# Optimization experiments

Hardware: AMD Instinct MI355X
Metric: run time of the kernel (lower is better)

## Reference

```python
import jax, jax.numpy as jnp
import numpy as np


def _patch_points(P):
    # replicates: meshgrid(y,x,z, indexing='ij'); points = cat([zz, yy, xx], -1).reshape(-1,3)
    lin = jnp.linspace(-1.0, 1.0, P)
    a, b, c = jnp.meshgrid(lin, lin, lin, indexing='ij')  # all identical linspaces
    pts = jnp.stack([c, b, a], axis=-1).reshape(-1, 3)     # (P^3, 3)
    return pts


def _proj_locations(points, angles):
    # Tomographic projection geometry (generate_projections_location):
    # rotate points about the detector-vertical axis and keep in-plane coords.
    # points: (N,3); angles: (A,) radians. Returns (A, N, 2) grid coords (x, y)
    # in grid_sample convention (last dim: x indexes width, y indexes height).
    p0 = points[:, 0]
    p1 = points[:, 1]
    p2 = points[:, 2]
    c = jnp.cos(angles)[:, None]   # (A,1)
    s = jnp.sin(angles)[:, None]
    gx = p0[None, :] * c + p2[None, :] * s          # (A, N)
    gy = jnp.broadcast_to(p1[None, :], gx.shape)    # (A, N)
    return jnp.stack([gx, gy], axis=-1)             # (A, N, 2)


def _bilinear_sample(img, grid):
    # img: (C,H,W); grid: (N,2) in [-1,1], align_corners=True, padding zeros.
    C, H, W = img.shape
    ix = (grid[:, 0] + 1.0) * 0.5 * (W - 1)
    iy = (grid[:, 1] + 1.0) * 0.5 * (H - 1)
    ix0 = jnp.floor(ix)
    iy0 = jnp.floor(iy)
    ix1 = ix0 + 1.0
    iy1 = iy0 + 1.0
    wx1 = ix - ix0
    wx0 = 1.0 - wx1
    wy1 = iy - iy0
    wy0 = 1.0 - wy1

    def corner(iyc, ixc, w):
        valid = (ixc >= 0) & (ixc <= W - 1) & (iyc >= 0) & (iyc <= H - 1)
        xi = jnp.clip(ixc, 0, W - 1).astype(jnp.int32)
        yi = jnp.clip(iyc, 0, H - 1).astype(jnp.int32)
        return img[:, yi, xi] * (w * valid)[None, :]   # (C,N)

    return (corner(iy0, ix0, wy0 * wx0) + corner(iy0, ix1, wy0 * wx1)
            + corner(iy1, ix0, wy1 * wx0) + corner(iy1, ix1, wy1 * wx1))


def setup_inputs() -> dict:
    key = jax.random.key(0)
    k1, k2 = jax.random.split(key)
    B, A, P = 128, 121, 33
    x = jax.random.normal(k1, (B, A, P, P), dtype=jnp.float32)
    angles = jax.random.uniform(k2, (1, A), dtype=jnp.float32,
                                minval=0.0, maxval=2.0 * np.pi)
    return {"x": x, "angles": angles}


def reference(x, angles):
    B, A, P, _ = x.shape
    pts = _patch_points(P)                       # (P^3, 3)
    grids = _proj_locations(pts, angles[0])      # (A, P^3, 2)
    xs = jnp.transpose(x, (1, 0, 2, 3))          # (A, B, P, P)

    def body(acc, inp):
        xi, gi = inp                             # (B,P,P), (P^3,2)
        return acc + _bilinear_sample(xi, gi), None

    acc0 = jnp.zeros((B, P * P * P), dtype=x.dtype)
    acc, _ = jax.lax.scan(body, acc0, (xs, grids))
    x_fbp = acc.reshape(B, P, P, P) / A
    return x_fbp
```

## Files before the change

kernel.cpp:

```cpp
#include <hip/hip_runtime.h>
#include <hip/hip_fp16.h>
#include <math.h>


#define PDIM 33
#define PP   1089
#define A_   121
#define K_   3993
#define KP   4032
#define MP   1152
#define MT2  18
#define NT2  66
#define OUTB 35937

typedef _Float16 f16x8 __attribute__((ext_vector_type(8)));
typedef float    f32x4 __attribute__((ext_vector_type(4)));

typedef __attribute__((address_space(1))) const unsigned int* gp_t;
typedef __attribute__((address_space(3))) unsigned int*       lp_t;


__global__ __launch_bounds__(128)
void wfill_kernel(const float* __restrict__ angles, __half* __restrict__ W)
{
    const int n = blockIdx.x;
    const int t = threadIdx.x;
    __half* row = W + (size_t)n * KP;
    for (int e = t; e < KP; e += 128) row[e] = __float2half_rn(0.0f);
    __syncthreads();
    if (n >= PP || t >= A_) return;
    const int j  = t;
    const int i0 = n / PDIM;
    const int i2 = n - i0 * PDIM;
    float s, c;
    sincosf(angles[j], &s, &c);
    float ix = fmaf((float)(i2 - 16), c, fmaf((float)(i0 - 16), s, 16.0f));
    float fl = floorf(ix);
    int   k0 = (int)fl;
    float w1 = ix - fl;
    float w0 = 1.0f - w1;
    __half* seg = row + j * PDIM;
    if (k0 >= 0     && k0 < PDIM)     seg[k0]     = __float2half_rn(w0);
    if (k0 + 1 >= 0 && k0 + 1 < PDIM) seg[k0 + 1] = __float2half_rn(w1);
}

__global__ __launch_bounds__(256)
void xt_kernel(const float* __restrict__ x, __half* __restrict__ Xt)
{
    const int n  = blockIdx.x;
    const int i1 = n >> 7;
    const int b  = n & 127;
    const float* src = x + (size_t)b * (A_ * PP) + (size_t)i1 * PDIM;
    unsigned int* dst = (unsigned int*)(Xt + (size_t)n * KP);
    for (int e = threadIdx.x; e < KP / 2; e += 256) {
        int kk0 = 2 * e, kk1 = 2 * e + 1;
        float v0 = 0.0f, v1 = 0.0f;
        if (kk0 < K_) {
            int j = kk0 / PDIM, k = kk0 - j * PDIM;
            v0 = src[(size_t)j * PP + k];
        }
        if (kk1 < K_) {
            int j = kk1 / PDIM, k = kk1 - j * PDIM;
            v1 = src[(size_t)j * PP + k];
        }
        dst[e] = __builtin_bit_cast(unsigned int,
                     __builtin_amdgcn_cvt_pkrtz(v0, v1));
    }
}

__global__ __launch_bounds__(256)
void gemm_kernel(const __half* __restrict__ W, const __half* __restrict__ Xt,
                 float* __restrict__ out, float invA)
{
    __shared__ _Float16 As[64 * 64];
    __shared__ _Float16 Bs[64 * 64];

    const int blk   = blockIdx.x;
    const int tileN = blk / MT2;
    const int tileM = blk - tileN * MT2;
    const int t     = threadIdx.x;
    const int lane  = t & 63;
    const int wave  = t >> 6;
    const int warpM = wave >> 1;
    const int warpN = wave & 1;
    const int quad  = lane >> 4;
    const int l15   = lane & 15;

    f32x4 acc[2][2] = {};

    const __half* Ab = W  + (size_t)(tileM * 64) * KP;
    const __half* Bb = Xt + (size_t)(tileN * 64) * KP;

    int srow[2], ssego[2];
#pragma unroll
    for (int i = 0; i < 2; ++i) {
        int cidx = t + i * 256;
        int row  = cidx >> 3;
        int seg  = cidx & 7;
        srow[i]  = row;
        ssego[i] = (seg ^ (row & 7)) * 8;
    }

    int arow[2], brow[2];
#pragma unroll
    for (int s = 0; s < 2; ++s) {
        arow[s] = warpM * 32 + s * 16 + l15;
        brow[s] = warpN * 32 + s * 16 + l15;
    }

    for (int kb = 0; kb < KP; kb += 64) {
        __syncthreads();
#pragma unroll
        for (int i = 0; i < 2; ++i) {
            const __half* ga = Ab + (size_t)srow[i] * KP + kb + ssego[i];
            const __half* gb = Bb + (size_t)srow[i] * KP + kb + ssego[i];
            __builtin_amdgcn_global_load_lds((gp_t)(const void*)ga,
                (lp_t)(void*)&As[(t + i * 256) * 8], 16, 0, 0);
            __builtin_amdgcn_global_load_lds((gp_t)(const void*)gb,
                (lp_t)(void*)&Bs[(t + i * 256) * 8], 16, 0, 0);
        }
        __syncthreads();

        f16x8 af[2][2], bf[2][2];
#pragma unroll
        for (int h = 0; h < 2; ++h) {
#pragma unroll
            for (int s = 0; s < 2; ++s) {
                int ks = h * 4 + quad;
                af[h][s] = *(const f16x8*)&As[arow[s] * 64 + ((ks ^ (arow[s] & 7)) * 8)];
                bf[h][s] = *(const f16x8*)&Bs[brow[s] * 64 + ((ks ^ (brow[s] & 7)) * 8)];
            }
        }
#pragma unroll
        for (int h = 0; h < 2; ++h)
#pragma unroll
            for (int ms = 0; ms < 2; ++ms)
#pragma unroll
                for (int ns = 0; ns < 2; ++ns)
                    acc[ms][ns] = __builtin_amdgcn_mfma_f32_16x16x32_f16(
                        af[h][ms], bf[h][ns], acc[ms][ns], 0, 0, 0);
    }

#pragma unroll
    for (int ns = 0; ns < 2; ++ns) {
        int nglob = tileN * 64 + warpN * 32 + ns * 16 + l15;
        int i1 = nglob >> 7;
        int b  = nglob & 127;
        float* ob = out + (size_t)b * OUTB + (size_t)i1 * PDIM;
#pragma unroll
        for (int ms = 0; ms < 2; ++ms) {
#pragma unroll
            for (int r = 0; r < 4; ++r) {
                int m = tileM * 64 + warpM * 32 + ms * 16 + quad * 4 + r;
                if (m < PP) {
                    int i0 = m / PDIM;
                    int i2 = m - i0 * PDIM;
                    ob[(size_t)i0 * PP + i2] = acc[ms][ns][r] * invA;
                }
            }
        }
    }
}


#define ROWW 47
#define PADL 7
#define BLK  384
#define NV   3
#define GRID 1280

typedef _Float16 h2v __attribute__((ext_vector_type(2)));

#if defined(__has_builtin)
#if __has_builtin(__builtin_amdgcn_fractf)
#define FRACTF(x) __builtin_amdgcn_fractf(x)
#endif
#endif
#ifndef FRACTF
#define FRACTF(x) ((x) - floorf(x))
#endif

__device__ __forceinline__ float fdot2u(unsigned int a, unsigned int b, float c)
{
    return __builtin_amdgcn_fdot2(__builtin_bit_cast(h2v, a),
                                  __builtin_bit_cast(h2v, b), c, false);
}

__global__ __launch_bounds__(BLK)
void fbp_adjoint_kernel(const float* __restrict__ x,
                        const float* __restrict__ angles,
                        float* __restrict__ out,
                        int nslice, float invA)
{
    __shared__ unsigned int dr[A_ * ROWW];
    __shared__ float2       cs_lds[A_];

    const int t = threadIdx.x;
    for (int j = t; j < A_; j += BLK) {
        float s, c;
        sincosf(angles[j], &s, &c);
        cs_lds[j] = make_float2(c, s);
    }

    float u0[NV], u2[NV];
#pragma unroll
    for (int nn = 0; nn < NV; ++nn) {
        int n  = t + nn * BLK;
        int nc = (n < PP) ? n : (PP - 1);
        int q0 = nc / PDIM;
        int q2 = nc - q0 * PDIM;
        u0[nn] = (float)(q0 - 16);
        u2[nn] = (float)(q2 - 16);
    }

    for (int slice = blockIdx.x; slice < nslice; slice += GRID) {
        if (slice != (int)blockIdx.x) __syncthreads();
        const int hb = slice / PDIM;
        const int i1 = slice - hb * PDIM;
        const int b0 = 2 * hb;
        const float* r0 = x + (size_t)b0 * (A_ * PP) + (size_t)i1 * PDIM;
        const float* r1 = r0 + (size_t)(A_ * PP);
        for (int e = t; e < A_ * ROWW; e += BLK) {
            int j = e / ROWW;
            int p = e - j * ROWW;
            int k = p - PADL;
            float f0 = 0.0f, f1 = 0.0f;
            if (k >= 0 && k < PDIM) {
                size_t o = (size_t)j * PP + k;
                f0 = r0[o];
                f1 = r1[o];
            }
            dr[e] = __builtin_bit_cast(unsigned int,
                        __halves2half2(__float2half_rn(f0), __float2half_rn(f1)));
        }
        __syncthreads();

        float a0[NV] = {0.0f, 0.0f, 0.0f};
        float a1[NV] = {0.0f, 0.0f, 0.0f};
#pragma unroll 2
        for (int j = 0; j < A_; ++j) {
            float2 cj = cs_lds[j];
            const unsigned int* base = &dr[j * ROWW];
#pragma unroll
            for (int nn = 0; nn < NV; ++nn) {
                float ixp = fmaf(u2[nn], cj.x, fmaf(u0[nn], cj.y, 23.0f));
                int   kp  = (int)ixp;
                float w1  = FRACTF(ixp);
                unsigned int wp = __builtin_bit_cast(unsigned int,
                                    __builtin_amdgcn_cvt_pkrtz(1.0f - w1, w1));
                unsigned int d0 = base[kp];
                unsigned int d1 = base[kp + 1];
                unsigned int p0 = __builtin_amdgcn_perm(d1, d0, 0x05040100u);
                unsigned int p1 = __builtin_amdgcn_perm(d1, d0, 0x07060302u);
                a0[nn] = fdot2u(p0, wp, a0[nn]);
                a1[nn] = fdot2u(p1, wp, a1[nn]);
            }
        }

        float* ob0 = out + (size_t)b0 * OUTB + (size_t)i1 * PDIM;
        float* ob1 = ob0 + (size_t)OUTB;
#pragma unroll
        for (int nn = 0; nn < NV; ++nn) {
            int n = t + nn * BLK;
            if (n < PP) {
                int q0 = n / PDIM;
                int q2 = n - q0 * PDIM;
                size_t o = (size_t)q0 * PP + q2;
                ob0[o] = a0[nn] * invA;
                ob1[o] = a1[nn] * invA;
            }
        }
    }
}


extern "C" void kernel_launch(void* const* d_in, const int* in_sizes, int n_in,
                              void* d_out, int out_size, void* d_ws, size_t ws_size,
                              hipStream_t stream)
{
    const float* x      = (const float*)d_in[0];
    const float* angles = (const float*)d_in[1];
    float* out          = (float*)d_out;

    const int A = in_sizes[1];
    const int B = in_sizes[0] / (A * PP);
    const float invA = 1.0f / (float)A;

    const size_t wBytes  = (size_t)MP * KP * sizeof(__half);
    const size_t xtBytes = (size_t)(PDIM * B) * KP * sizeof(__half);

    if (ws_size >= wBytes + xtBytes && A == A_ && B == 128) {
        __half* W  = (__half*)d_ws;
        __half* Xt = (__half*)((char*)d_ws + wBytes);
        wfill_kernel<<<MP, 128, 0, stream>>>(angles, W);
        xt_kernel<<<PDIM * B, 256, 0, stream>>>(x, Xt);
        gemm_kernel<<<NT2 * MT2, 256, 0, stream>>>(W, Xt, out, invA);
    } else {
        const int nslice = (B / 2) * PDIM;
        dim3 grid(GRID < nslice ? GRID : nslice);
        fbp_adjoint_kernel<<<grid, BLK, 0, stream>>>(x, angles, out,
                                                     nslice, invA);
    }
}
```

Measured before the change: 191.5 us.

## Double-buffer GEMM LDS tiles and merge prep kernels into one launch

Result: slower. 199.0 us (+4.0%).

```diff
diff --git a/kernel.cpp b/kernel.cpp
--- a/kernel.cpp
+++ b/kernel.cpp
@@ -20,51 +20,54 @@
 typedef __attribute__((address_space(3))) unsigned int*       lp_t;
 
 
-__global__ __launch_bounds__(128)
-void wfill_kernel(const float* __restrict__ angles, __half* __restrict__ W)
-{
-    const int n = blockIdx.x;
-    const int t = threadIdx.x;
-    __half* row = W + (size_t)n * KP;
-    for (int e = t; e < KP; e += 128) row[e] = __float2half_rn(0.0f);
-    __syncthreads();
-    if (n >= PP || t >= A_) return;
-    const int j  = t;
-    const int i0 = n / PDIM;
-    const int i2 = n - i0 * PDIM;
-    float s, c;
-    sincosf(angles[j], &s, &c);
-    float ix = fmaf((float)(i2 - 16), c, fmaf((float)(i0 - 16), s, 16.0f));
-    float fl = floorf(ix);
-    int   k0 = (int)fl;
-    float w1 = ix - fl;
-    float w0 = 1.0f - w1;
-    __half* seg = row + j * PDIM;
-    if (k0 >= 0     && k0 < PDIM)     seg[k0]     = __float2half_rn(w0);
-    if (k0 + 1 >= 0 && k0 + 1 < PDIM) seg[k0 + 1] = __float2half_rn(w1);
-}
-
 __global__ __launch_bounds__(256)
-void xt_kernel(const float* __restrict__ x, __half* __restrict__ Xt)
-{
-    const int n  = blockIdx.x;
-    const int i1 = n >> 7;
-    const int b  = n & 127;
-    const float* src = x + (size_t)b * (A_ * PP) + (size_t)i1 * PDIM;
-    unsigned int* dst = (unsigned int*)(Xt + (size_t)n * KP);
-    for (int e = threadIdx.x; e < KP / 2; e += 256) {
-        int kk0 = 2 * e, kk1 = 2 * e + 1;
-        float v0 = 0.0f, v1 = 0.0f;
-        if (kk0 < K_) {
-            int j = kk0 / PDIM, k = kk0 - j * PDIM;
-            v0 = src[(size_t)j * PP + k];
-        }
-        if (kk1 < K_) {
-            int j = kk1 / PDIM, k = kk1 - j * PDIM;
-            v1 = src[(size_t)j * PP + k];
-        }
-        dst[e] = __builtin_bit_cast(unsigned int,
-                     __builtin_amdgcn_cvt_pkrtz(v0, v1));
+void prep_kernel(const float* __restrict__ x, const float* __restrict__ angles,
+                 __half* __restrict__ Xt, __half* __restrict__ W)
+{
+    const int blk = blockIdx.x;
+    const int t   = threadIdx.x;
+
+    if (blk < PDIM * 128) {
+        const int n  = blk;
+        const int i1 = n >> 7;
+        const int b  = n & 127;
+        const float* src = x + (size_t)b * (A_ * PP) + (size_t)i1 * PDIM;
+        unsigned int* dst = (unsigned int*)(Xt + (size_t)n * KP);
+        for (int e = t; e < KP / 2; e += 256) {
+            int kk0 = 2 * e, kk1 = 2 * e + 1;
+            float v0 = 0.0f, v1 = 0.0f;
+            if (kk0 < K_) {
+                int j = kk0 / PDIM, k = kk0 - j * PDIM;
+                v0 = src[(size_t)j * PP + k];
+            }
+            if (kk1 < K_) {
+                int j = kk1 / PDIM, k = kk1 - j * PDIM;
+                v1 = src[(size_t)j * PP + k];
+            }
+            dst[e] = __builtin_bit_cast(unsigned int,
+                         __builtin_amdgcn_cvt_pkrtz(v0, v1));
+        }
+    } else {
+        const int n = blk - PDIM * 128;
+        __half* row = W + (size_t)n * KP;
+        int4 zz = make_int4(0, 0, 0, 0);
+        for (int e = t; e < KP / 8; e += 256)
+            ((int4*)row)[e] = zz;
+        __syncthreads();
+        if (n >= PP || t >= A_) return;
+        const int j  = t;
+        const int i0 = n / PDIM;
+        const int i2 = n - i0 * PDIM;
+        float s, c;
+        sincosf(angles[j], &s, &c);
+        float ix = fmaf((float)(i2 - 16), c, fmaf((float)(i0 - 16), s, 16.0f));
+        float fl = floorf(ix);
+        int   k0 = (int)fl;
+        float w1 = ix - fl;
+        float w0 = 1.0f - w1;
+        __half* seg = row + j * PDIM;
+        if (k0 >= 0     && k0 < PDIM)     seg[k0]     = __float2half_rn(w0);
+        if (k0 + 1 >= 0 && k0 + 1 < PDIM) seg[k0 + 1] = __float2half_rn(w1);
     }
 }
 
@@ -72,8 +75,8 @@
 void gemm_kernel(const __half* __restrict__ W, const __half* __restrict__ Xt,
                  float* __restrict__ out, float invA)
 {
-    __shared__ _Float16 As[64 * 64];
-    __shared__ _Float16 Bs[64 * 64];
+    __shared__ _Float16 As[2][64 * 64];
+    __shared__ _Float16 Bs[2][64 * 64];
 
     const int blk   = blockIdx.x;
     const int tileN = blk / MT2;
@@ -108,27 +111,29 @@
         brow[s] = warpN * 32 + s * 16 + l15;
     }
 
-    for (int kb = 0; kb < KP; kb += 64) {
-        __syncthreads();
+    auto stage = [&](int sel, int kb) {
 #pragma unroll
         for (int i = 0; i < 2; ++i) {
             const __half* ga = Ab + (size_t)srow[i] * KP + kb + ssego[i];
             const __half* gb = Bb + (size_t)srow[i] * KP + kb + ssego[i];
             __builtin_amdgcn_global_load_lds((gp_t)(const void*)ga,
-                (lp_t)(void*)&As[(t + i * 256) * 8], 16, 0, 0);
+                (lp_t)(void*)&As[sel][(t + i * 256) * 8], 16, 0, 0);
             __builtin_amdgcn_global_load_lds((gp_t)(const void*)gb,
-                (lp_t)(void*)&Bs[(t + i * 256) * 8], 16, 0, 0);
-        }
-        __syncthreads();
-
+                (lp_t)(void*)&Bs[sel][(t + i * 256) * 8], 16, 0, 0);
+        }
+    };
+
+    auto compute = [&](int sel) {
         f16x8 af[2][2], bf[2][2];
 #pragma unroll
         for (int h = 0; h < 2; ++h) {
 #pragma unroll
             for (int s = 0; s < 2; ++s) {
                 int ks = h * 4 + quad;
-                af[h][s] = *(const f16x8*)&As[arow[s] * 64 + ((ks ^ (arow[s] & 7)) * 8)];
-                bf[h][s] = *(const f16x8*)&Bs[brow[s] * 64 + ((ks ^ (brow[s] & 7)) * 8)];
+                af[h][s] = *(const f16x8*)
+                    &As[sel][arow[s] * 64 + ((ks ^ (arow[s] & 7)) * 8)];
+                bf[h][s] = *(const f16x8*)
+                    &Bs[sel][brow[s] * 64 + ((ks ^ (brow[s] & 7)) * 8)];
             }
         }
 #pragma unroll
@@ -139,7 +144,32 @@
                 for (int ns = 0; ns < 2; ++ns)
                     acc[ms][ns] = __builtin_amdgcn_mfma_f32_16x16x32_f16(
                         af[h][ms], bf[h][ns], acc[ms][ns], 0, 0, 0);
-    }
+    };
+
+    stage(0, 0);
+    for (int kb = 64; kb + 64 < KP; kb += 128) {
+        stage(1, kb);
+        asm volatile("s_waitcnt vmcnt(4)" ::: "memory");
+        __builtin_amdgcn_s_barrier();
+        asm volatile("" ::: "memory");
+        compute(0);
+        asm volatile("" ::: "memory");
+        __builtin_amdgcn_s_barrier();
+        asm volatile("" ::: "memory");
+
+        stage(0, kb + 64);
+        asm volatile("s_waitcnt vmcnt(4)" ::: "memory");
+        __builtin_amdgcn_s_barrier();
+        asm volatile("" ::: "memory");
+        compute(1);
+        asm volatile("" ::: "memory");
+        __builtin_amdgcn_s_barrier();
+        asm volatile("" ::: "memory");
+    }
+    asm volatile("s_waitcnt vmcnt(0)" ::: "memory");
+    __builtin_amdgcn_s_barrier();
+    asm volatile("" ::: "memory");
+    compute(0);
 
 #pragma unroll
     for (int ns = 0; ns < 2; ++ns) {
@@ -292,8 +322,7 @@
     if (ws_size >= wBytes + xtBytes && A == A_ && B == 128) {
         __half* W  = (__half*)d_ws;
         __half* Xt = (__half*)((char*)d_ws + wBytes);
-        wfill_kernel<<<MP, 128, 0, stream>>>(angles, W);
-        xt_kernel<<<PDIM * B, 256, 0, stream>>>(x, Xt);
+        prep_kernel<<<PDIM * B + MP, 256, 0, stream>>>(x, angles, Xt, W);
         gemm_kernel<<<NT2 * MT2, 256, 0, stream>>>(W, Xt, out, invA);
     } else {
         const int nslice = (B / 2) * PDIM;
```

## Split GEMM K dimension in two, merge prep kernels, add reduction pass

Applied to the files above, without the earlier changes.

Measured after the change: 211.3 us. +10.4%, slower.

```diff
diff --git a/kernel.cpp b/kernel.cpp
--- a/kernel.cpp
+++ b/kernel.cpp
@@ -8,6 +8,7 @@
 #define A_   121
 #define K_   3993
 #define KP   4032
+#define KSPL 2048
 #define MP   1152
 #define MT2  18
 #define NT2  66
@@ -20,62 +21,73 @@
 typedef __attribute__((address_space(3))) unsigned int*       lp_t;
 
 
-__global__ __launch_bounds__(128)
-void wfill_kernel(const float* __restrict__ angles, __half* __restrict__ W)
-{
-    const int n = blockIdx.x;
-    const int t = threadIdx.x;
-    __half* row = W + (size_t)n * KP;
-    for (int e = t; e < KP; e += 128) row[e] = __float2half_rn(0.0f);
-    __syncthreads();
-    if (n >= PP || t >= A_) return;
-    const int j  = t;
-    const int i0 = n / PDIM;
-    const int i2 = n - i0 * PDIM;
-    float s, c;
-    sincosf(angles[j], &s, &c);
-    float ix = fmaf((float)(i2 - 16), c, fmaf((float)(i0 - 16), s, 16.0f));
-    float fl = floorf(ix);
-    int   k0 = (int)fl;
-    float w1 = ix - fl;
-    float w0 = 1.0f - w1;
-    __half* seg = row + j * PDIM;
-    if (k0 >= 0     && k0 < PDIM)     seg[k0]     = __float2half_rn(w0);
-    if (k0 + 1 >= 0 && k0 + 1 < PDIM) seg[k0 + 1] = __float2half_rn(w1);
-}
-
 __global__ __launch_bounds__(256)
-void xt_kernel(const float* __restrict__ x, __half* __restrict__ Xt)
-{
-    const int n  = blockIdx.x;
-    const int i1 = n >> 7;
-    const int b  = n & 127;
-    const float* src = x + (size_t)b * (A_ * PP) + (size_t)i1 * PDIM;
-    unsigned int* dst = (unsigned int*)(Xt + (size_t)n * KP);
-    for (int e = threadIdx.x; e < KP / 2; e += 256) {
-        int kk0 = 2 * e, kk1 = 2 * e + 1;
-        float v0 = 0.0f, v1 = 0.0f;
-        if (kk0 < K_) {
-            int j = kk0 / PDIM, k = kk0 - j * PDIM;
-            v0 = src[(size_t)j * PP + k];
-        }
-        if (kk1 < K_) {
-            int j = kk1 / PDIM, k = kk1 - j * PDIM;
-            v1 = src[(size_t)j * PP + k];
-        }
-        dst[e] = __builtin_bit_cast(unsigned int,
-                     __builtin_amdgcn_cvt_pkrtz(v0, v1));
+void prep_kernel(const float* __restrict__ x, const float* __restrict__ angles,
+                 __half* __restrict__ Xt, __half* __restrict__ W)
+{
+    const int blk = blockIdx.x;
+    const int t   = threadIdx.x;
+
+    if (blk < PDIM * 128) {
+        const int n  = blk;
+        const int i1 = n >> 7;
+        const int b  = n & 127;
+        const float* src = x + (size_t)b * (A_ * PP) + (size_t)i1 * PDIM;
+        unsigned int* dst = (unsigned int*)(Xt + (size_t)n * KP);
+        for (int e = t; e < KP / 2; e += 256) {
+            int kk0 = 2 * e, kk1 = 2 * e + 1;
+            float v0 = 0.0f, v1 = 0.0f;
+            if (kk0 < K_) {
+                int j = kk0 / PDIM, k = kk0 - j * PDIM;
+                v0 = src[(size_t)j * PP + k];
+            }
+            if (kk1 < K_) {
+                int j = kk1 / PDIM, k = kk1 - j * PDIM;
+                v1 = src[(size_t)j * PP + k];
+            }
+            dst[e] = __builtin_bit_cast(unsigned int,
+                         __builtin_amdgcn_cvt_pkrtz(v0, v1));
+        }
+    } else {
+        const int n = blk - PDIM * 128;
+        __half* row = W + (size_t)n * KP;
+        int4 zz = make_int4(0, 0, 0, 0);
+        for (int e = t; e < KP / 8; e += 256)
+            ((int4*)row)[e] = zz;
+        __syncthreads();
+        if (n >= PP || t >= A_) return;
+        const int j  = t;
+        const int i0 = n / PDIM;
+        const int i2 = n - i0 * PDIM;
+        float s, c;
+        sincosf(angles[j], &s, &c);
+        float ix = fmaf((float)(i2 - 16), c, fmaf((float)(i0 - 16), s, 16.0f));
+        float fl = floorf(ix);
+        int   k0 = (int)fl;
+        float w1 = ix - fl;
+        float w0 = 1.0f - w1;
+        __half* seg = row + j * PDIM;
+        if (k0 >= 0     && k0 < PDIM)     seg[k0]     = __float2half_rn(w0);
+        if (k0 + 1 >= 0 && k0 + 1 < PDIM) seg[k0 + 1] = __float2half_rn(w1);
     }
 }
 
 __global__ __launch_bounds__(256)
 void gemm_kernel(const __half* __restrict__ W, const __half* __restrict__ Xt,
-                 float* __restrict__ out, float invA)
+                 float* __restrict__ out, float* __restrict__ part,
+                 float scale)
 {
     __shared__ _Float16 As[64 * 64];
     __shared__ _Float16 Bs[64 * 64];
 
-    const int blk   = blockIdx.x;
+    int blk = blockIdx.x;
+    int kb0 = 0, kb1 = KP;
+    float* dst = out;
+    if (part) {
+        if (blk >= MT2 * NT2) { blk -= MT2 * NT2; dst = part; kb0 = KSPL; }
+        else                  { kb1 = KSPL; }
+    }
+
     const int tileN = blk / MT2;
     const int tileM = blk - tileN * MT2;
     const int t     = threadIdx.x;
@@ -108,7 +120,7 @@
         brow[s] = warpN * 32 + s * 16 + l15;
     }
 
-    for (int kb = 0; kb < KP; kb += 64) {
+    for (int kb = kb0; kb < kb1; kb += 64) {
         __syncthreads();
 #pragma unroll
         for (int i = 0; i < 2; ++i) {
@@ -146,7 +158,7 @@
         int nglob = tileN * 64 + warpN * 32 + ns * 16 + l15;
         int i1 = nglob >> 7;
         int b  = nglob & 127;
-        float* ob = out + (size_t)b * OUTB + (size_t)i1 * PDIM;
+        float* ob = dst + (size_t)b * OUTB + (size_t)i1 * PDIM;
 #pragma unroll
         for (int ms = 0; ms < 2; ++ms) {
 #pragma unroll
@@ -155,10 +167,29 @@
                 if (m < PP) {
                     int i0 = m / PDIM;
                     int i2 = m - i0 * PDIM;
-                    ob[(size_t)i0 * PP + i2] = acc[ms][ns][r] * invA;
+                    ob[(size_t)i0 * PP + i2] = acc[ms][ns][r] * scale;
                 }
             }
         }
+    }
+}
+
+__global__ __launch_bounds__(256)
+void reduce_kernel(float* __restrict__ out, const float* __restrict__ part,
+                   float invA)
+{
+    const int n4 = (128 * OUTB) / 4;
+    float4* o4 = (float4*)out;
+    const float4* p4 = (const float4*)part;
+    for (int e = blockIdx.x * 256 + threadIdx.x; e < n4;
+         e += gridDim.x * 256) {
+        float4 a = o4[e];
+        float4 b = p4[e];
+        a.x = (a.x + b.x) * invA;
+        a.y = (a.y + b.y) * invA;
+        a.z = (a.z + b.z) * invA;
+        a.w = (a.w + b.w) * invA;
+        o4[e] = a;
     }
 }
 
@@ -288,13 +319,20 @@
 
     const size_t wBytes  = (size_t)MP * KP * sizeof(__half);
     const size_t xtBytes = (size_t)(PDIM * B) * KP * sizeof(__half);
-
-    if (ws_size >= wBytes + xtBytes && A == A_ && B == 128) {
+    const size_t pBytes  = (size_t)128 * OUTB * sizeof(float);
+
+    if (ws_size >= wBytes + xtBytes + pBytes && A == A_ && B == 128) {
         __half* W  = (__half*)d_ws;
         __half* Xt = (__half*)((char*)d_ws + wBytes);
-        wfill_kernel<<<MP, 128, 0, stream>>>(angles, W);
-        xt_kernel<<<PDIM * B, 256, 0, stream>>>(x, Xt);
-        gemm_kernel<<<NT2 * MT2, 256, 0, stream>>>(W, Xt, out, invA);
+        float*  P  = (float*)((char*)d_ws + wBytes + xtBytes);
+        prep_kernel<<<PDIM * B + MP, 256, 0, stream>>>(x, angles, Xt, W);
+        gemm_kernel<<<2 * NT2 * MT2, 256, 0, stream>>>(W, Xt, out, P, 1.0f);
+        reduce_kernel<<<2048, 256, 0, stream>>>(out, P, invA);
+    } else if (ws_size >= wBytes + xtBytes && A == A_ && B == 128) {
+        __half* W  = (__half*)d_ws;
+        __half* Xt = (__half*)((char*)d_ws + wBytes);
+        prep_kernel<<<PDIM * B + MP, 256, 0, stream>>>(x, angles, Xt, W);
+        gemm_kernel<<<NT2 * MT2, 256, 0, stream>>>(W, Xt, out, nullptr, invA);
     } else {
         const int nslice = (B / 2) * PDIM;
         dim3 grid(GRID < nslice ? GRID : nslice);
```

## Merge prep kernels into one launch and double GEMM K-tile to 128

Applied to the files above, without the earlier changes.

Result: slower. 196.6 us (+2.7%).

```diff
diff --git a/kernel.cpp b/kernel.cpp
--- a/kernel.cpp
+++ b/kernel.cpp
@@ -7,7 +7,8 @@
 #define PP   1089
 #define A_   121
 #define K_   3993
-#define KP   4032
+#define KP   4096
+#define BK   128
 #define MP   1152
 #define MT2  18
 #define NT2  66
@@ -20,51 +21,54 @@
 typedef __attribute__((address_space(3))) unsigned int*       lp_t;
 
 
-__global__ __launch_bounds__(128)
-void wfill_kernel(const float* __restrict__ angles, __half* __restrict__ W)
-{
-    const int n = blockIdx.x;
-    const int t = threadIdx.x;
-    __half* row = W + (size_t)n * KP;
-    for (int e = t; e < KP; e += 128) row[e] = __float2half_rn(0.0f);
-    __syncthreads();
-    if (n >= PP || t >= A_) return;
-    const int j  = t;
-    const int i0 = n / PDIM;
-    const int i2 = n - i0 * PDIM;
-    float s, c;
-    sincosf(angles[j], &s, &c);
-    float ix = fmaf((float)(i2 - 16), c, fmaf((float)(i0 - 16), s, 16.0f));
-    float fl = floorf(ix);
-    int   k0 = (int)fl;
-    float w1 = ix - fl;
-    float w0 = 1.0f - w1;
-    __half* seg = row + j * PDIM;
-    if (k0 >= 0     && k0 < PDIM)     seg[k0]     = __float2half_rn(w0);
-    if (k0 + 1 >= 0 && k0 + 1 < PDIM) seg[k0 + 1] = __float2half_rn(w1);
-}
-
 __global__ __launch_bounds__(256)
-void xt_kernel(const float* __restrict__ x, __half* __restrict__ Xt)
-{
-    const int n  = blockIdx.x;
-    const int i1 = n >> 7;
-    const int b  = n & 127;
-    const float* src = x + (size_t)b * (A_ * PP) + (size_t)i1 * PDIM;
-    unsigned int* dst = (unsigned int*)(Xt + (size_t)n * KP);
-    for (int e = threadIdx.x; e < KP / 2; e += 256) {
-        int kk0 = 2 * e, kk1 = 2 * e + 1;
-        float v0 = 0.0f, v1 = 0.0f;
-        if (kk0 < K_) {
-            int j = kk0 / PDIM, k = kk0 - j * PDIM;
-            v0 = src[(size_t)j * PP + k];
-        }
-        if (kk1 < K_) {
-            int j = kk1 / PDIM, k = kk1 - j * PDIM;
-            v1 = src[(size_t)j * PP + k];
-        }
-        dst[e] = __builtin_bit_cast(unsigned int,
-                     __builtin_amdgcn_cvt_pkrtz(v0, v1));
+void prep_kernel(const float* __restrict__ x, const float* __restrict__ angles,
+                 __half* __restrict__ Xt, __half* __restrict__ W)
+{
+    const int blk = blockIdx.x;
+    const int t   = threadIdx.x;
+
+    if (blk < PDIM * 128) {
+        const int n  = blk;
+        const int i1 = n >> 7;
+        const int b  = n & 127;
+        const float* src = x + (size_t)b * (A_ * PP) + (size_t)i1 * PDIM;
+        unsigned int* dst = (unsigned int*)(Xt + (size_t)n * KP);
+        for (int e = t; e < KP / 2; e += 256) {
+            int kk0 = 2 * e, kk1 = 2 * e + 1;
+            float v0 = 0.0f, v1 = 0.0f;
+            if (kk0 < K_) {
+                int j = kk0 / PDIM, k = kk0 - j * PDIM;
+                v0 = src[(size_t)j * PP + k];
+            }
+            if (kk1 < K_) {
+                int j = kk1 / PDIM, k = kk1 - j * PDIM;
+                v1 = src[(size_t)j * PP + k];
+            }
+            dst[e] = __builtin_bit_cast(unsigned int,
+                         __builtin_amdgcn_cvt_pkrtz(v0, v1));
+        }
+    } else {
+        const int n = blk - PDIM * 128;
+        __half* row = W + (size_t)n * KP;
+        int4 zz = make_int4(0, 0, 0, 0);
+        for (int e = t; e < KP / 8; e += 256)
+            ((int4*)row)[e] = zz;
+        __syncthreads();
+        if (n >= PP || t >= A_) return;
+        const int j  = t;
+        const int i0 = n / PDIM;
+        const int i2 = n - i0 * PDIM;
+        float s, c;
+        sincosf(angles[j], &s, &c);
+        float ix = fmaf((float)(i2 - 16), c, fmaf((float)(i0 - 16), s, 16.0f));
+        float fl = floorf(ix);
+        int   k0 = (int)fl;
+        float w1 = ix - fl;
+        float w0 = 1.0f - w1;
+        __half* seg = row + j * PDIM;
+        if (k0 >= 0     && k0 < PDIM)     seg[k0]     = __float2half_rn(w0);
+        if (k0 + 1 >= 0 && k0 + 1 < PDIM) seg[k0 + 1] = __float2half_rn(w1);
     }
 }
 
@@ -72,8 +76,8 @@
 void gemm_kernel(const __half* __restrict__ W, const __half* __restrict__ Xt,
                  float* __restrict__ out, float invA)
 {
-    __shared__ _Float16 As[64 * 64];
-    __shared__ _Float16 Bs[64 * 64];
+    __shared__ _Float16 As[64 * BK];
+    __shared__ _Float16 Bs[64 * BK];
 
     const int blk   = blockIdx.x;
     const int tileN = blk / MT2;
@@ -91,14 +95,14 @@
     const __half* Ab = W  + (size_t)(tileM * 64) * KP;
     const __half* Bb = Xt + (size_t)(tileN * 64) * KP;
 
-    int srow[2], ssego[2];
-#pragma unroll
-    for (int i = 0; i < 2; ++i) {
+    int srow[4], ssego[4];
+#pragma unroll
+    for (int i = 0; i < 4; ++i) {
         int cidx = t + i * 256;
-        int row  = cidx >> 3;
-        int seg  = cidx & 7;
+        int row  = cidx >> 4;
+        int seg  = cidx & 15;
         srow[i]  = row;
-        ssego[i] = (seg ^ (row & 7)) * 8;
+        ssego[i] = (seg ^ (row & 15)) * 8;
     }
 
     int arow[2], brow[2];
@@ -108,10 +112,10 @@
         brow[s] = warpN * 32 + s * 16 + l15;
     }
 
-    for (int kb = 0; kb < KP; kb += 64) {
+    for (int kb = 0; kb < KP; kb += BK) {
         __syncthreads();
 #pragma unroll
-        for (int i = 0; i < 2; ++i) {
+        for (int i = 0; i < 4; ++i) {
             const __half* ga = Ab + (size_t)srow[i] * KP + kb + ssego[i];
             const __half* gb = Bb + (size_t)srow[i] * KP + kb + ssego[i];
             __builtin_amdgcn_global_load_lds((gp_t)(const void*)ga,
@@ -121,18 +125,20 @@
         }
         __syncthreads();
 
-        f16x8 af[2][2], bf[2][2];
-#pragma unroll
-        for (int h = 0; h < 2; ++h) {
+        f16x8 af[4][2], bf[4][2];
+#pragma unroll
+        for (int h = 0; h < 4; ++h) {
 #pragma unroll
             for (int s = 0; s < 2; ++s) {
                 int ks = h * 4 + quad;
-                af[h][s] = *(const f16x8*)&As[arow[s] * 64 + ((ks ^ (arow[s] & 7)) * 8)];
-                bf[h][s] = *(const f16x8*)&Bs[brow[s] * 64 + ((ks ^ (brow[s] & 7)) * 8)];
-            }
-        }
-#pragma unroll
-        for (int h = 0; h < 2; ++h)
+                af[h][s] = *(const f16x8*)
+                    &As[arow[s] * BK + ((ks ^ (arow[s] & 15)) * 8)];
+                bf[h][s] = *(const f16x8*)
+                    &Bs[brow[s] * BK + ((ks ^ (brow[s] & 15)) * 8)];
+            }
+        }
+#pragma unroll
+        for (int h = 0; h < 4; ++h)
 #pragma unroll
             for (int ms = 0; ms < 2; ++ms)
 #pragma unroll
@@ -292,8 +298,7 @@
     if (ws_size >= wBytes + xtBytes && A == A_ && B == 128) {
         __half* W  = (__half*)d_ws;
         __half* Xt = (__half*)((char*)d_ws + wBytes);
-        wfill_kernel<<<MP, 128, 0, stream>>>(angles, W);
-        xt_kernel<<<PDIM * B, 256, 0, stream>>>(x, Xt);
+        prep_kernel<<<PDIM * B + MP, 256, 0, stream>>>(x, angles, Xt, W);
         gemm_kernel<<<NT2 * MT2, 256, 0, stream>>>(W, Xt, out, invA);
     } else {
         const int nslice = (B / 2) * PDIM;
```
